# Kernel optimization log

Measured on AMD Instinct MI355X. Metric: run time of the kernel, lower is better.

Reference implementation:

```python
import jax, jax.numpy as jnp
import numpy as np

NUM_HEADS = 16
THETA = 10000.0

def _apply_rope(x, positions):
    # x: [B, H, S, dh] with interleaved pairs; positions: [B, S] int
    dh = x.shape[-1]
    inv_freq = THETA ** (-jnp.arange(0, dh, 2, dtype=jnp.float32) / dh)  # [dh/2]
    ang = positions.astype(jnp.float32)[:, None, :, None] * inv_freq  # [B,1,S,dh/2]
    cos, sin = jnp.cos(ang), jnp.sin(ang)
    x1, x2 = x[..., 0::2], x[..., 1::2]
    out_even = x1 * cos - x2 * sin
    out_odd = x1 * sin + x2 * cos
    return jnp.stack([out_even, out_odd], axis=-1).reshape(x.shape)

def setup_inputs() -> dict:
    B, S, D = 2, 2048, 2048
    key = jax.random.key(0)
    ks = jax.random.split(key, 5)
    scale = 0.02
    inp = {
        'in_features': jax.random.normal(ks[0], (B, S, D), dtype=jnp.float32),
        'token_positions': jnp.broadcast_to(jnp.arange(S, dtype=jnp.int32), (B, S)),
        'mask': jnp.tril(jnp.ones((S, S), dtype=bool)),
        'q_proj_weight': jax.random.normal(ks[1], (D, D), dtype=jnp.float32) * scale,
        'k_proj_weight': jax.random.normal(ks[2], (D, D), dtype=jnp.float32) * scale,
        'v_proj_weight': jax.random.normal(ks[3], (D, D), dtype=jnp.float32) * scale,
        'o_proj_weight': jax.random.normal(ks[4], (D, D), dtype=jnp.float32) * scale,
    }
    return inp

def reference(in_features, token_positions, mask, q_proj_weight, k_proj_weight, v_proj_weight, o_proj_weight):
    B, S, d_in = in_features.shape
    d_k = q_proj_weight.shape[0]
    d_v = v_proj_weight.shape[0]
    H = NUM_HEADS
    dk_head, dv_head = d_k // H, d_v // H
    Q = jnp.einsum('bsd,kd->bsk', in_features, q_proj_weight).reshape(B, S, H, dk_head).transpose(0, 2, 1, 3)
    K = jnp.einsum('bsd,kd->bsk', in_features, k_proj_weight).reshape(B, S, H, dk_head).transpose(0, 2, 1, 3)
    V = jnp.einsum('bsd,vd->bsv', in_features, v_proj_weight).reshape(B, S, H, dv_head).transpose(0, 2, 1, 3)
    Q = _apply_rope(Q, token_positions)
    K = _apply_rope(K, token_positions)
    scores = jnp.einsum('bhqd,bhkd->bhqk', Q, K) / jnp.sqrt(jnp.float32(dk_head))
    scores = jnp.where(mask[None, None, :, :], scores, jnp.finfo(scores.dtype).min)
    attn = jax.nn.softmax(scores, axis=-1)
    out = jnp.einsum('bhqk,bhkd->bhqd', attn, V)  # [B,H,S,dv_head]
    out = out.transpose(0, 2, 1, 3).reshape(B, S, d_v)
    return jnp.einsum('bsv,mv->bsm', out, o_proj_weight)
```

## Files before the change

kernel.cpp:

```cpp
#include <hip/hip_runtime.h>
#include <hip/hip_bf16.h>
#include <cstdint>

typedef __bf16 bf16_t;
typedef __bf16 bf16x8 __attribute__((ext_vector_type(8)));
typedef __bf16 bf16x4 __attribute__((ext_vector_type(4)));
typedef float  f32x4  __attribute__((ext_vector_type(4)));

#define B_  2
#define S_  2048
#define D_  2048
#define H_  16
#define DH_ 128

__device__ __forceinline__ void gload_lds16(const bf16_t* g, bf16_t* l) {
    __builtin_amdgcn_global_load_lds(
        (const __attribute__((address_space(1))) void*)g,
        (__attribute__((address_space(3))) void*)l, 16, 0, 0);
}

__global__ __launch_bounds__(256) void cast_bf16_k(const float* __restrict__ in,
                                                   bf16_t* __restrict__ out) {
    long i = ((long)blockIdx.x * blockDim.x + threadIdx.x) * 4;
    float4 v = *(const float4*)(in + i);
    bf16x4 o = {(bf16_t)v.x, (bf16_t)v.y, (bf16_t)v.z, (bf16_t)v.w};
    *(bf16x4*)(out + i) = o;
}

template<bool C_BF16>
__global__ __launch_bounds__(256)
void gemm_nt(const bf16_t* __restrict__ A, int lda,
             const bf16_t* __restrict__ B, int ldb,
             void* __restrict__ Cp, int ldc, int coff, int K) {
    __shared__ bf16_t As[128 * 32];
    __shared__ bf16_t Bs[128 * 32];
    const int tid  = threadIdx.x;
    const int wave = tid >> 6;
    const int lane = tid & 63;
    const long bm = (long)blockIdx.y * 128;
    const long bn = (long)blockIdx.x * 128;

    const int srow0 = wave * 16 + (lane >> 2);
    const int srow1 = (4 + wave) * 16 + (lane >> 2);
    const int scol  = (lane & 3) * 8;
    const bf16_t* Ag0 = A + (bm + srow0) * (long)lda + scol;
    const bf16_t* Ag1 = A + (bm + srow1) * (long)lda + scol;
    const bf16_t* Bg0 = B + (bn + srow0) * (long)ldb + scol;
    const bf16_t* Bg1 = B + (bn + srow1) * (long)ldb + scol;
    bf16_t* Al0 = &As[wave * 512];
    bf16_t* Al1 = &As[(4 + wave) * 512];
    bf16_t* Bl0 = &Bs[wave * 512];
    bf16_t* Bl1 = &Bs[(4 + wave) * 512];

    const int wr = (wave >> 1) * 64;
    const int wc = (wave & 1) * 64;
    const int fr = lane & 15;
    const int ko = (lane >> 4) * 8;

    f32x4 acc[4][4] = {};

    for (int k0 = 0; k0 < K; k0 += 32) {
        gload_lds16(Ag0 + k0, Al0);
        gload_lds16(Ag1 + k0, Al1);
        gload_lds16(Bg0 + k0, Bl0);
        gload_lds16(Bg1 + k0, Bl1);
        __syncthreads();
        bf16x8 a[4], b[4];
#pragma unroll
        for (int i = 0; i < 4; ++i)
            a[i] = *(const bf16x8*)&As[(wr + i * 16 + fr) * 32 + ko];
#pragma unroll
        for (int j = 0; j < 4; ++j)
            b[j] = *(const bf16x8*)&Bs[(wc + j * 16 + fr) * 32 + ko];
#pragma unroll
        for (int i = 0; i < 4; ++i)
#pragma unroll
            for (int j = 0; j < 4; ++j)
                acc[i][j] = __builtin_amdgcn_mfma_f32_16x16x32_bf16(a[i], b[j], acc[i][j], 0, 0, 0);
        __syncthreads();
    }

#pragma unroll
    for (int i = 0; i < 4; ++i) {
        long r0 = bm + wr + i * 16 + (lane >> 4) * 4;
#pragma unroll
        for (int j = 0; j < 4; ++j) {
            long cc = bn + wc + j * 16 + (lane & 15) + coff;
#pragma unroll
            for (int v = 0; v < 4; ++v) {
                if (C_BF16)
                    ((bf16_t*)Cp)[(r0 + v) * (long)ldc + cc] = (bf16_t)acc[i][j][v];
                else
                    ((float*)Cp)[(r0 + v) * (long)ldc + cc] = acc[i][j][v];
            }
        }
    }
}

__global__ __launch_bounds__(256)
void rope_qk_k(bf16_t* __restrict__ Qp, bf16_t* __restrict__ Kp,
               const int* __restrict__ pos) {
    int t = blockIdx.x * 256 + threadIdx.x;
    int i = t & 63;
    int h = (t >> 6) & 15;
    int s = (t >> 10) & 2047;
    int b = t >> 21;
    long a = ((long)(b * S_ + s)) * D_ + h * DH_ + 2 * i;
    float p = (float)pos[b * S_ + s];
    float invf = exp2f(-(float)i * 0.20762050593045702f);
    float ang = p * invf;
    float sn, cs;
    sincosf(ang, &sn, &cs);
    float q1 = (float)Qp[a], q2 = (float)Qp[a + 1];
    Qp[a]     = (bf16_t)(q1 * cs - q2 * sn);
    Qp[a + 1] = (bf16_t)(q1 * sn + q2 * cs);
    float k1 = (float)Kp[a], k2 = (float)Kp[a + 1];
    Kp[a]     = (bf16_t)(k1 * cs - k2 * sn);
    Kp[a + 1] = (bf16_t)(k1 * sn + k2 * cs);
}

__global__ __launch_bounds__(256)
void transpose_v_k(const bf16_t* __restrict__ Vp, bf16_t* __restrict__ Vt) {
    __shared__ bf16_t tile[64][80];
    int t = threadIdx.x;
    int bh = blockIdx.z;
    int b = bh >> 4, h = bh & 15;
    long s0 = (long)blockIdx.x * 64;
    int d0 = blockIdx.y * 64;
    const bf16_t* src = Vp + ((long)b * S_ + s0) * D_ + h * DH_ + d0;
#pragma unroll
    for (int p = 0; p < 2; ++p) {
        int r = (t >> 3) + p * 32;
        int c = (t & 7) * 8;
        *(bf16x8*)&tile[r][c] = *(const bf16x8*)&src[(long)r * D_ + c];
    }
    __syncthreads();
    bf16_t* dst = Vt + ((long)bh * DH_ + d0) * S_ + s0;
#pragma unroll
    for (int p = 0; p < 2; ++p) {
        int d = (t >> 3) + p * 32;
        int c = (t & 7) * 8;
        bf16x8 v;
#pragma unroll
        for (int e = 0; e < 8; ++e) v[e] = tile[c + e][d];
        *(bf16x8*)&dst[(long)d * S_ + c] = v;
    }
}

__device__ __forceinline__ bf16x8 ldsw(const bf16_t* p, int row, int ecol) {
    return *(const bf16x8*)(p + row * 128 + (ecol ^ ((row & 7) << 3)));
}

__global__ __launch_bounds__(512, 1)
void flash_attn_k(const bf16_t* __restrict__ Q, const bf16_t* __restrict__ K,
                  const bf16_t* __restrict__ Vt, bf16_t* __restrict__ O) {
    __shared__ bf16_t Ksh[128 * 128];
    __shared__ bf16_t Vsh[128 * 128];
    __shared__ bf16_t Psh[128 * 128];

    const int tid  = threadIdx.x;
    const int w    = tid >> 6;
    const int lane = tid & 63;
    const int fr   = lane & 15;
    const int hi   = lane >> 4;
    const int hi8  = hi * 8;
    const int hi4  = hi * 4;
    const int w16  = w * 16;

    const int bid = blockIdx.x;
    const int qi  = 15 - (bid >> 5);
    const int bh  = bid & 31;
    const int b   = bh >> 4;
    const int h   = bh & 15;
    const long bS   = (long)b * S_;
    const int  hoff = h * DH_;
    const long vbase = (long)bh * DH_;

#pragma unroll
    for (int p = 0; p < 4; ++p) {
        int idx = p * 512 + tid;
        int row = idx >> 4;
        int sl  = (idx & 15) ^ (row & 7);
        gload_lds16(Q + (bS + qi * 128 + row) * D_ + hoff + sl * 8,
                    &Psh[(p * 512 + w * 64) * 8]);
    }
    __syncthreads();

    bf16x8 qfrag[4];
#pragma unroll
    for (int kk = 0; kk < 4; ++kk)
        qfrag[kk] = ldsw(Psh, w16 + fr, kk * 32 + hi8);

    f32x4 o[8] = {};
    float m_run[4] = {-3.0e38f, -3.0e38f, -3.0e38f, -3.0e38f};
    float l_run[4] = {};

    const float SC = 0.08838834764831845f * 1.4426950408889634f;

    for (int kt = 0; kt <= qi; ++kt) {
#pragma unroll
        for (int p = 0; p < 4; ++p) {
            int idx = p * 512 + tid;
            int row = idx >> 4;
            int sl  = (idx & 15) ^ (row & 7);
            gload_lds16(K  + (bS + kt * 128 + row) * D_ + hoff + sl * 8,
                        &Ksh[(p * 512 + w * 64) * 8]);
            gload_lds16(Vt + (vbase + row) * S_ + kt * 128 + sl * 8,
                        &Vsh[(p * 512 + w * 64) * 8]);
        }
        __syncthreads();

        f32x4 sc[8];
#pragma unroll
        for (int j = 0; j < 8; ++j) {
            f32x4 z = {};
#pragma unroll
            for (int kk = 0; kk < 4; ++kk)
                z = __builtin_amdgcn_mfma_f32_16x16x32_bf16(
                        qfrag[kk], ldsw(Ksh, j * 16 + fr, kk * 32 + hi8), z, 0, 0, 0);
            sc[j] = z;
        }

        const bool diag = (kt == qi);
#pragma unroll
        for (int j = 0; j < 8; ++j)
#pragma unroll
            for (int v = 0; v < 4; ++v) {
                float x = sc[j][v] * SC;
                if (diag && (j * 16 + fr > w16 + hi4 + v)) x = -3.0e38f;
                sc[j][v] = x;
            }

        float fsc[4];
#pragma unroll
        for (int v = 0; v < 4; ++v) {
            float m = fmaxf(fmaxf(fmaxf(sc[0][v], sc[1][v]), fmaxf(sc[2][v], sc[3][v])),
                            fmaxf(fmaxf(sc[4][v], sc[5][v]), fmaxf(sc[6][v], sc[7][v])));
            m = fmaxf(m, __shfl_xor(m, 1));
            m = fmaxf(m, __shfl_xor(m, 2));
            m = fmaxf(m, __shfl_xor(m, 4));
            m = fmaxf(m, __shfl_xor(m, 8));
            float mn = fmaxf(m_run[v], m);
            fsc[v] = exp2f(m_run[v] - mn);
            m_run[v] = mn;
            l_run[v] *= fsc[v];
        }
#pragma unroll
        for (int j2 = 0; j2 < 8; ++j2)
#pragma unroll
            for (int v = 0; v < 4; ++v) o[j2][v] *= fsc[v];

#pragma unroll
        for (int j = 0; j < 8; ++j)
#pragma unroll
            for (int v = 0; v < 4; ++v) {
                float p = exp2f(sc[j][v] - m_run[v]);
                l_run[v] += p;
                int row = w16 + hi4 + v;
                int col = j * 16 + fr;
                Psh[row * 128 + (col ^ ((row & 7) << 3))] = (bf16_t)p;
            }

        asm volatile("s_waitcnt lgkmcnt(0)" ::: "memory");

        bf16x8 pa[4];
#pragma unroll
        for (int kk = 0; kk < 4; ++kk)
            pa[kk] = ldsw(Psh, w16 + fr, kk * 32 + hi8);
#pragma unroll
        for (int j2 = 0; j2 < 8; ++j2)
#pragma unroll
            for (int kk = 0; kk < 4; ++kk)
                o[j2] = __builtin_amdgcn_mfma_f32_16x16x32_bf16(
                            pa[kk], ldsw(Vsh, j2 * 16 + fr, kk * 32 + hi8), o[j2], 0, 0, 0);

        __syncthreads();
    }

#pragma unroll
    for (int v = 0; v < 4; ++v) {
        float l = l_run[v];
        l += __shfl_xor(l, 1);
        l += __shfl_xor(l, 2);
        l += __shfl_xor(l, 4);
        l += __shfl_xor(l, 8);
        l_run[v] = 1.0f / l;
    }
    const long orow = bS + qi * 128 + w16 + hi4;
#pragma unroll
    for (int j2 = 0; j2 < 8; ++j2)
#pragma unroll
        for (int v = 0; v < 4; ++v)
            O[(orow + v) * D_ + hoff + j2 * 16 + fr] = (bf16_t)(o[j2][v] * l_run[v]);
}

extern "C" void kernel_launch(void* const* d_in, const int* in_sizes, int n_in,
                              void* d_out, int out_size, void* d_ws, size_t ws_size,
                              hipStream_t stream) {
    const float* in_features = (const float*)d_in[0];
    const int*   positions   = (const int*)d_in[1];
    const float* Wq = (const float*)d_in[3];
    const float* Wk = (const float*)d_in[4];
    const float* Wv = (const float*)d_in[5];
    const float* Wo = (const float*)d_in[6];
    float* out = (float*)d_out;

    const size_t SZ_X = (size_t)B_ * S_ * D_ * 2;
    const size_t SZ_W = (size_t)D_ * D_ * 2;
    if (ws_size < SZ_X * 5 + SZ_W * 4) return;

    char* w = (char*)d_ws;
    bf16_t* Xb  = (bf16_t*)w;             w += SZ_X;
    bf16_t* Wqb = (bf16_t*)w;             w += SZ_W;
    bf16_t* Wkb = (bf16_t*)w;             w += SZ_W;
    bf16_t* Wvb = (bf16_t*)w;             w += SZ_W;
    bf16_t* Wob = (bf16_t*)w;             w += SZ_W;
    bf16_t* Qp  = (bf16_t*)w;             w += SZ_X;
    bf16_t* Kp  = (bf16_t*)w;             w += SZ_X;
    bf16_t* Vp  = (bf16_t*)w;             w += SZ_X;
    bf16_t* Vt  = (bf16_t*)w;             w += SZ_X;
    bf16_t* AttnOut = Vp;

    cast_bf16_k<<<8192, 256, 0, stream>>>(in_features, Xb);
    cast_bf16_k<<<4096, 256, 0, stream>>>(Wq, Wqb);
    cast_bf16_k<<<4096, 256, 0, stream>>>(Wk, Wkb);
    cast_bf16_k<<<4096, 256, 0, stream>>>(Wv, Wvb);
    cast_bf16_k<<<4096, 256, 0, stream>>>(Wo, Wob);

    gemm_nt<true><<<dim3(16, 32), 256, 0, stream>>>(Xb, D_, Wqb, D_, Qp, D_, 0, D_);
    gemm_nt<true><<<dim3(16, 32), 256, 0, stream>>>(Xb, D_, Wkb, D_, Kp, D_, 0, D_);
    gemm_nt<true><<<dim3(16, 32), 256, 0, stream>>>(Xb, D_, Wvb, D_, Vp, D_, 0, D_);

    rope_qk_k<<<16384, 256, 0, stream>>>(Qp, Kp, positions);
    transpose_v_k<<<dim3(32, 2, 32), 256, 0, stream>>>(Vp, Vt);

    flash_attn_k<<<512, 512, 0, stream>>>(Qp, Kp, Vt, AttnOut);

    gemm_nt<false><<<dim3(16, 32), 256, 0, stream>>>(AttnOut, D_, Wob, D_, out, D_, 0, D_);
}
```

Before: 476.9 us.

## Fuse QKV GEMM, merge casts, vectorize RoPE, double-buffer attention K/V

Merges the five cast launches into one kernel and the three projection GEMMs into a single GEMM over a concatenated QKV weight with a 6144-wide output. Adds a workgroup index swizzle to the GEMM to improve L2 reuse. RoPE now handles eight elements per thread with vector loads and the fast __sincosf. The flash attention kernel double-buffers K/V tiles in LDS, prefetching the next tile with partial vmcnt waits in place of full syncthreads. This doubles the K/V LDS footprint, and the fast sincos loses accuracy at large angles.

Result: faster. 439.0 us (-7.9%).

```diff
diff --git a/kernel.cpp b/kernel.cpp
--- a/kernel.cpp
+++ b/kernel.cpp
@@ -12,6 +12,7 @@
 #define D_  2048
 #define H_  16
 #define DH_ 128
+#define LDQ 6144
 
 __device__ __forceinline__ void gload_lds16(const bf16_t* g, bf16_t* l) {
     __builtin_amdgcn_global_load_lds(
@@ -19,26 +20,42 @@
         (__attribute__((address_space(3))) void*)l, 16, 0, 0);
 }
 
-__global__ __launch_bounds__(256) void cast_bf16_k(const float* __restrict__ in,
-                                                   bf16_t* __restrict__ out) {
-    long i = ((long)blockIdx.x * blockDim.x + threadIdx.x) * 4;
-    float4 v = *(const float4*)(in + i);
+__global__ __launch_bounds__(256)
+void cast_all_k(const float* __restrict__ X,  const float* __restrict__ Wq,
+                const float* __restrict__ Wk, const float* __restrict__ Wv,
+                const float* __restrict__ Wo,
+                bf16_t* __restrict__ Xb, bf16_t* __restrict__ Wqkv,
+                bf16_t* __restrict__ Wob) {
+    long bid = blockIdx.x;
+    const float* src; bf16_t* dst; long off;
+    if      (bid <  8192) { src = X;  dst = Xb;             off = bid;         }
+    else if (bid < 12288) { src = Wq; dst = Wqkv;           off = bid - 8192;  }
+    else if (bid < 16384) { src = Wk; dst = Wqkv + 4194304; off = bid - 12288; }
+    else if (bid < 20480) { src = Wv; dst = Wqkv + 8388608; off = bid - 16384; }
+    else                  { src = Wo; dst = Wob;            off = bid - 20480; }
+    long i = (off * 256 + threadIdx.x) * 4;
+    float4 v = *(const float4*)(src + i);
     bf16x4 o = {(bf16_t)v.x, (bf16_t)v.y, (bf16_t)v.z, (bf16_t)v.w};
-    *(bf16x4*)(out + i) = o;
+    *(bf16x4*)(dst + i) = o;
 }
 
 template<bool C_BF16>
 __global__ __launch_bounds__(256)
 void gemm_nt(const bf16_t* __restrict__ A, int lda,
              const bf16_t* __restrict__ B, int ldb,
-             void* __restrict__ Cp, int ldc, int coff, int K) {
+             void* __restrict__ Cp, int ldc, int K) {
     __shared__ bf16_t As[128 * 32];
     __shared__ bf16_t Bs[128 * 32];
     const int tid  = threadIdx.x;
     const int wave = tid >> 6;
     const int lane = tid & 63;
-    const long bm = (long)blockIdx.y * 128;
-    const long bn = (long)blockIdx.x * 128;
+
+    const int ntx = gridDim.x;
+    const int nwg = ntx * gridDim.y;
+    const int lin = blockIdx.y * ntx + blockIdx.x;
+    const int swz = (lin & 7) * (nwg >> 3) + (lin >> 3);
+    const long bm = (long)(swz / ntx) * 128;
+    const long bn = (long)(swz % ntx) * 128;
 
     const int srow0 = wave * 16 + (lane >> 2);
     const int srow1 = (4 + wave) * 16 + (lane >> 2);
@@ -85,7 +102,7 @@
         long r0 = bm + wr + i * 16 + (lane >> 4) * 4;
 #pragma unroll
         for (int j = 0; j < 4; ++j) {
-            long cc = bn + wc + j * 16 + (lane & 15) + coff;
+            long cc = bn + wc + j * 16 + (lane & 15);
 #pragma unroll
             for (int v = 0; v < 4; ++v) {
                 if (C_BF16)
@@ -98,41 +115,49 @@
 }
 
 __global__ __launch_bounds__(256)
-void rope_qk_k(bf16_t* __restrict__ Qp, bf16_t* __restrict__ Kp,
-               const int* __restrict__ pos) {
+void rope_qk_k(bf16_t* __restrict__ QKV, const int* __restrict__ pos) {
     int t = blockIdx.x * 256 + threadIdx.x;
-    int i = t & 63;
-    int h = (t >> 6) & 15;
-    int s = (t >> 10) & 2047;
-    int b = t >> 21;
-    long a = ((long)(b * S_ + s)) * D_ + h * DH_ + 2 * i;
+    int g = t & 15;
+    int h = (t >> 4) & 15;
+    int s = (t >> 8) & 2047;
+    int b = t >> 19;
+    long qa = ((long)(b * S_ + s)) * LDQ + h * DH_ + g * 8;
+    long ka = qa + D_;
     float p = (float)pos[b * S_ + s];
-    float invf = exp2f(-(float)i * 0.20762050593045702f);
-    float ang = p * invf;
-    float sn, cs;
-    sincosf(ang, &sn, &cs);
-    float q1 = (float)Qp[a], q2 = (float)Qp[a + 1];
-    Qp[a]     = (bf16_t)(q1 * cs - q2 * sn);
-    Qp[a + 1] = (bf16_t)(q1 * sn + q2 * cs);
-    float k1 = (float)Kp[a], k2 = (float)Kp[a + 1];
-    Kp[a]     = (bf16_t)(k1 * cs - k2 * sn);
-    Kp[a + 1] = (bf16_t)(k1 * sn + k2 * cs);
+    bf16x8 q = *(bf16x8*)(QKV + qa);
+    bf16x8 k = *(bf16x8*)(QKV + ka);
+#pragma unroll
+    for (int e = 0; e < 4; ++e) {
+        int i = g * 4 + e;
+        float invf = exp2f(-(float)i * 0.20762050593045702f);
+        float ang = p * invf;
+        float sn, cs;
+        __sincosf(ang, &sn, &cs);
+        float q1 = (float)q[2 * e], q2 = (float)q[2 * e + 1];
+        q[2 * e]     = (bf16_t)(q1 * cs - q2 * sn);
+        q[2 * e + 1] = (bf16_t)(q1 * sn + q2 * cs);
+        float k1 = (float)k[2 * e], k2 = (float)k[2 * e + 1];
+        k[2 * e]     = (bf16_t)(k1 * cs - k2 * sn);
+        k[2 * e + 1] = (bf16_t)(k1 * sn + k2 * cs);
+    }
+    *(bf16x8*)(QKV + qa) = q;
+    *(bf16x8*)(QKV + ka) = k;
 }
 
 __global__ __launch_bounds__(256)
-void transpose_v_k(const bf16_t* __restrict__ Vp, bf16_t* __restrict__ Vt) {
+void transpose_v_k(const bf16_t* __restrict__ QKV, bf16_t* __restrict__ Vt) {
     __shared__ bf16_t tile[64][80];
     int t = threadIdx.x;
     int bh = blockIdx.z;
     int b = bh >> 4, h = bh & 15;
     long s0 = (long)blockIdx.x * 64;
     int d0 = blockIdx.y * 64;
-    const bf16_t* src = Vp + ((long)b * S_ + s0) * D_ + h * DH_ + d0;
+    const bf16_t* src = QKV + ((long)b * S_ + s0) * LDQ + 2 * D_ + h * DH_ + d0;
 #pragma unroll
     for (int p = 0; p < 2; ++p) {
         int r = (t >> 3) + p * 32;
         int c = (t & 7) * 8;
-        *(bf16x8*)&tile[r][c] = *(const bf16x8*)&src[(long)r * D_ + c];
+        *(bf16x8*)&tile[r][c] = *(const bf16x8*)&src[(long)r * LDQ + c];
     }
     __syncthreads();
     bf16_t* dst = Vt + ((long)bh * DH_ + d0) * S_ + s0;
@@ -152,10 +177,10 @@
 }
 
 __global__ __launch_bounds__(512, 1)
-void flash_attn_k(const bf16_t* __restrict__ Q, const bf16_t* __restrict__ K,
-                  const bf16_t* __restrict__ Vt, bf16_t* __restrict__ O) {
-    __shared__ bf16_t Ksh[128 * 128];
-    __shared__ bf16_t Vsh[128 * 128];
+void flash_attn_k(const bf16_t* __restrict__ QKV, const bf16_t* __restrict__ Vt,
+                  bf16_t* __restrict__ O) {
+    __shared__ bf16_t Ksh[2][128 * 128];
+    __shared__ bf16_t Vsh[2][128 * 128];
     __shared__ bf16_t Psh[128 * 128];
 
     const int tid  = threadIdx.x;
@@ -173,7 +198,8 @@
     const int b   = bh >> 4;
     const int h   = bh & 15;
     const long bS   = (long)b * S_;
-    const int  hoff = h * DH_;
+    const int  qoff = h * DH_;
+    const int  koff = D_ + h * DH_;
     const long vbase = (long)bh * DH_;
 
 #pragma unroll
@@ -181,10 +207,22 @@
         int idx = p * 512 + tid;
         int row = idx >> 4;
         int sl  = (idx & 15) ^ (row & 7);
-        gload_lds16(Q + (bS + qi * 128 + row) * D_ + hoff + sl * 8,
+        gload_lds16(QKV + (bS + qi * 128 + row) * (long)LDQ + qoff + sl * 8,
                     &Psh[(p * 512 + w * 64) * 8]);
     }
-    __syncthreads();
+#pragma unroll
+    for (int p = 0; p < 4; ++p) {
+        int idx = p * 512 + tid;
+        int row = idx >> 4;
+        int sl  = (idx & 15) ^ (row & 7);
+        gload_lds16(QKV + (bS + row) * (long)LDQ + koff + sl * 8,
+                    &Ksh[0][(p * 512 + w * 64) * 8]);
+        gload_lds16(Vt + (vbase + row) * S_ + sl * 8,
+                    &Vsh[0][(p * 512 + w * 64) * 8]);
+    }
+    asm volatile("s_waitcnt vmcnt(8)" ::: "memory");
+    __builtin_amdgcn_s_barrier();
+    asm volatile("" ::: "memory");
 
     bf16x8 qfrag[4];
 #pragma unroll
@@ -198,17 +236,24 @@
     const float SC = 0.08838834764831845f * 1.4426950408889634f;
 
     for (int kt = 0; kt <= qi; ++kt) {
-#pragma unroll
-        for (int p = 0; p < 4; ++p) {
-            int idx = p * 512 + tid;
-            int row = idx >> 4;
-            int sl  = (idx & 15) ^ (row & 7);
-            gload_lds16(K  + (bS + kt * 128 + row) * D_ + hoff + sl * 8,
-                        &Ksh[(p * 512 + w * 64) * 8]);
-            gload_lds16(Vt + (vbase + row) * S_ + kt * 128 + sl * 8,
-                        &Vsh[(p * 512 + w * 64) * 8]);
+        const int buf = kt & 1;
+        if (kt < qi) {
+#pragma unroll
+            for (int p = 0; p < 4; ++p) {
+                int idx = p * 512 + tid;
+                int row = idx >> 4;
+                int sl  = (idx & 15) ^ (row & 7);
+                gload_lds16(QKV + (bS + (kt + 1) * 128 + row) * (long)LDQ + koff + sl * 8,
+                            &Ksh[buf ^ 1][(p * 512 + w * 64) * 8]);
+                gload_lds16(Vt + (vbase + row) * S_ + (kt + 1) * 128 + sl * 8,
+                            &Vsh[buf ^ 1][(p * 512 + w * 64) * 8]);
+            }
+            asm volatile("s_waitcnt vmcnt(8)" ::: "memory");
+        } else {
+            asm volatile("s_waitcnt vmcnt(0)" ::: "memory");
         }
-        __syncthreads();
+        __builtin_amdgcn_s_barrier();
+        asm volatile("" ::: "memory");
 
         f32x4 sc[8];
 #pragma unroll
@@ -217,7 +262,7 @@
 #pragma unroll
             for (int kk = 0; kk < 4; ++kk)
                 z = __builtin_amdgcn_mfma_f32_16x16x32_bf16(
-                        qfrag[kk], ldsw(Ksh, j * 16 + fr, kk * 32 + hi8), z, 0, 0, 0);
+                        qfrag[kk], ldsw(Ksh[buf], j * 16 + fr, kk * 32 + hi8), z, 0, 0, 0);
             sc[j] = z;
         }
 
@@ -262,6 +307,7 @@
             }
 
         asm volatile("s_waitcnt lgkmcnt(0)" ::: "memory");
+        __builtin_amdgcn_sched_barrier(0);
 
         bf16x8 pa[4];
 #pragma unroll
@@ -272,9 +318,11 @@
 #pragma unroll
             for (int kk = 0; kk < 4; ++kk)
                 o[j2] = __builtin_amdgcn_mfma_f32_16x16x32_bf16(
-                            pa[kk], ldsw(Vsh, j2 * 16 + fr, kk * 32 + hi8), o[j2], 0, 0, 0);
-
-        __syncthreads();
+                            pa[kk], ldsw(Vsh[buf], j2 * 16 + fr, kk * 32 + hi8), o[j2], 0, 0, 0);
+
+        asm volatile("" ::: "memory");
+        __builtin_amdgcn_s_barrier();
+        asm volatile("" ::: "memory");
     }
 
 #pragma unroll
@@ -291,7 +339,7 @@
     for (int j2 = 0; j2 < 8; ++j2)
 #pragma unroll
         for (int v = 0; v < 4; ++v)
-            O[(orow + v) * D_ + hoff + j2 * 16 + fr] = (bf16_t)(o[j2][v] * l_run[v]);
+            O[(orow + v) * D_ + qoff + j2 * 16 + fr] = (bf16_t)(o[j2][v] * l_run[v]);
 }
 
 extern "C" void kernel_launch(void* const* d_in, const int* in_sizes, int n_in,
@@ -305,36 +353,27 @@
     const float* Wo = (const float*)d_in[6];
     float* out = (float*)d_out;
 
-    const size_t SZ_X = (size_t)B_ * S_ * D_ * 2;
-    const size_t SZ_W = (size_t)D_ * D_ * 2;
-    if (ws_size < SZ_X * 5 + SZ_W * 4) return;
+    const size_t SZ_X   = (size_t)B_ * S_ * D_ * 2;
+    const size_t SZ_W   = (size_t)D_ * D_ * 2;
+    const size_t SZ_QKV = (size_t)B_ * S_ * LDQ * 2;
+    if (ws_size < SZ_X * 3 + SZ_W * 4 + SZ_QKV) return;
 
     char* w = (char*)d_ws;
-    bf16_t* Xb  = (bf16_t*)w;             w += SZ_X;
-    bf16_t* Wqb = (bf16_t*)w;             w += SZ_W;
-    bf16_t* Wkb = (bf16_t*)w;             w += SZ_W;
-    bf16_t* Wvb = (bf16_t*)w;             w += SZ_W;
-    bf16_t* Wob = (bf16_t*)w;             w += SZ_W;
-    bf16_t* Qp  = (bf16_t*)w;             w += SZ_X;
-    bf16_t* Kp  = (bf16_t*)w;             w += SZ_X;
-    bf16_t* Vp  = (bf16_t*)w;             w += SZ_X;
-    bf16_t* Vt  = (bf16_t*)w;             w += SZ_X;
-    bf16_t* AttnOut = Vp;
-
-    cast_bf16_k<<<8192, 256, 0, stream>>>(in_features, Xb);
-    cast_bf16_k<<<4096, 256, 0, stream>>>(Wq, Wqb);
-    cast_bf16_k<<<4096, 256, 0, stream>>>(Wk, Wkb);
-    cast_bf16_k<<<4096, 256, 0, stream>>>(Wv, Wvb);
-    cast_bf16_k<<<4096, 256, 0, stream>>>(Wo, Wob);
-
-    gemm_nt<true><<<dim3(16, 32), 256, 0, stream>>>(Xb, D_, Wqb, D_, Qp, D_, 0, D_);
-    gemm_nt<true><<<dim3(16, 32), 256, 0, stream>>>(Xb, D_, Wkb, D_, Kp, D_, 0, D_);
-    gemm_nt<true><<<dim3(16, 32), 256, 0, stream>>>(Xb, D_, Wvb, D_, Vp, D_, 0, D_);
-
-    rope_qk_k<<<16384, 256, 0, stream>>>(Qp, Kp, positions);
-    transpose_v_k<<<dim3(32, 2, 32), 256, 0, stream>>>(Vp, Vt);
-
-    flash_attn_k<<<512, 512, 0, stream>>>(Qp, Kp, Vt, AttnOut);
-
-    gemm_nt<false><<<dim3(16, 32), 256, 0, stream>>>(AttnOut, D_, Wob, D_, out, D_, 0, D_);
-}
+    bf16_t* Xb      = (bf16_t*)w;   w += SZ_X;
+    bf16_t* Wqkv    = (bf16_t*)w;   w += SZ_W * 3;
+    bf16_t* Wob     = (bf16_t*)w;   w += SZ_W;
+    bf16_t* QKV     = (bf16_t*)w;   w += SZ_QKV;
+    bf16_t* Vt      = (bf16_t*)w;   w += SZ_X;
+    bf16_t* AttnOut = (bf16_t*)w;   w += SZ_X;
+
+    cast_all_k<<<24576, 256, 0, stream>>>(in_features, Wq, Wk, Wv, Wo, Xb, Wqkv, Wob);
+
+    gemm_nt<true><<<dim3(48, 32), 256, 0, stream>>>(Xb, D_, Wqkv, D_, QKV, LDQ, D_);
+
+    rope_qk_k<<<4096, 256, 0, stream>>>(QKV, positions);
+    transpose_v_k<<<dim3(32, 2, 32), 256, 0, stream>>>(QKV, Vt);
+
+    flash_attn_k<<<512, 512, 0, stream>>>(QKV, Vt, AttnOut);
+
+    gemm_nt<false><<<dim3(16, 32), 256, 0, stream>>>(AttnOut, D_, Wob, D_, out, D_, D_);
+}
```
